# Kernel optimization log

Hardware: AMD Instinct MI355X
Metric: run time of the kernel (lower is better)

The kernel has to match this reference:

```python
import jax, jax.numpy as jnp
import numpy as np

D = 2048
H = 16
KV = 4
DH = D // H  # 128
REP = H // KV
ROPE_BASE = 10000.0


def _rope(x, pos):
    # x: (B, h, L, Dh), pos: (L,)
    half = x.shape[-1] // 2
    inv_freq = 1.0 / (ROPE_BASE ** (jnp.arange(0, half, dtype=jnp.float32) / half))
    ang = pos.astype(jnp.float32)[:, None] * inv_freq[None, :]          # (L, half)
    cos = jnp.concatenate([jnp.cos(ang), jnp.cos(ang)], axis=-1)        # (L, Dh)
    sin = jnp.concatenate([jnp.sin(ang), jnp.sin(ang)], axis=-1)
    x1, x2 = x[..., :half], x[..., half:]
    rot = jnp.concatenate([-x2, x1], axis=-1)
    return x * cos[None, None] + rot * sin[None, None]


def setup_inputs() -> dict:
    key = jax.random.key(0)
    ks = jax.random.split(key, 5)
    s = 1.0 / np.sqrt(D)
    return {
        "x": jax.random.normal(ks[0], (2, 2048, D), dtype=jnp.float32),
        "wq": jax.random.uniform(ks[1], (H * DH, D), jnp.float32, -s, s),
        "wk": jax.random.uniform(ks[2], (KV * DH, D), jnp.float32, -s, s),
        "wv": jax.random.uniform(ks[3], (KV * DH, D), jnp.float32, -s, s),
        "wo": jax.random.uniform(ks[4], (D, H * DH), jnp.float32, -s, s),
    }


def reference(x, wq, wk, wv, wo):
    B, T, _ = x.shape
    q = (x @ wq.T).reshape(B, T, H, DH).transpose(0, 2, 1, 3)    # (B,H,T,Dh)
    k = (x @ wk.T).reshape(B, T, KV, DH).transpose(0, 2, 1, 3)   # (B,KV,T,Dh)
    v = (x @ wv.T).reshape(B, T, KV, DH).transpose(0, 2, 1, 3)
    Tc = T  # no kv cache
    pos = jnp.arange(Tc)
    q = _rope(q, pos)
    k = _rope(k, pos)
    # GQA: repeat kv heads to match query heads
    k_full = jnp.repeat(k, REP, axis=1)                          # (B,H,Tc,Dh)
    v_full = jnp.repeat(v, REP, axis=1)
    scale = 1.0 / np.sqrt(DH)
    scores = jnp.einsum('bhtd,bhsd->bhts', q, k_full) * scale    # (B,H,T,Tc)
    row = jnp.arange(T)[:, None]
    col = jnp.arange(Tc)[None, :]
    causal = col <= row + (Tc - T)
    scores = jnp.where(causal[None, None], scores, -jnp.inf)
    attn = jax.nn.softmax(scores, axis=-1)
    out = jnp.einsum('bhts,bhsd->bhtd', attn, v_full)            # (B,H,T,Dh)
    out = out.transpose(0, 2, 1, 3).reshape(B, T, H * DH)
    return out @ wo.T
```

## Files before the change

kernel.cpp:

```cpp
#include <hip/hip_runtime.h>

typedef float f32x4 __attribute__((ext_vector_type(4)));
typedef short s16x8 __attribute__((ext_vector_type(8)));
typedef unsigned short u16;

__device__ __forceinline__ u16 f2bf(float f) {
    union { float f; unsigned u; } v; v.f = f;
    return (u16)((v.u + 0x7fffu + ((v.u >> 16) & 1u)) >> 16);
}
__device__ __forceinline__ float bf2f(u16 h) {
    union { unsigned u; float f; } v; v.u = ((unsigned)h) << 16;
    return v.f;
}
__device__ __forceinline__ float fast_exp2(float x) {
#if __has_builtin(__builtin_amdgcn_exp2f)
    return __builtin_amdgcn_exp2f(x);
#else
    return exp2f(x);
#endif
}

__device__ __forceinline__ void gload_lds16(const void* g, void* l) {
    __builtin_amdgcn_global_load_lds((__attribute__((address_space(1))) void*)g,
                                     (__attribute__((address_space(3))) void*)l, 16, 0, 0);
}

__global__ __launch_bounds__(256) void cvt_all(const float* __restrict__ x,  const float* __restrict__ wq,
                                               const float* __restrict__ wk, const float* __restrict__ wv,
                                               u16* __restrict__ xb, u16* __restrict__ wqkvb) {
    int u = blockIdx.x * 256 + threadIdx.x;
    const float* src;
    u16* dst;
    if (u < 1048576) { src = x + (size_t)u * 8; dst = xb + (size_t)u * 8; }
    else {
        int w = u - 1048576;
        dst = wqkvb + (size_t)w * 8;
        if (w < 524288)      src = wq + (size_t)w * 8;
        else if (w < 655360) src = wk + (size_t)(w - 524288) * 8;
        else                 src = wv + (size_t)(w - 655360) * 8;
    }
    const float4* p = (const float4*)src;
    float4 a = p[0], b = p[1];
    s16x8 o;
    o[0] = f2bf(a.x); o[1] = f2bf(a.y); o[2] = f2bf(a.z); o[3] = f2bf(a.w);
    o[4] = f2bf(b.x); o[5] = f2bf(b.y); o[6] = f2bf(b.z); o[7] = f2bf(b.w);
    *(s16x8*)dst = o;
}

__global__ __launch_bounds__(256) void cvt_kernel(const float* __restrict__ in,
                                                  u16* __restrict__ out, int n8) {
    int i = blockIdx.x * 256 + threadIdx.x;
    if (i >= n8) return;
    const float4* p = (const float4*)(in + (size_t)i * 8);
    float4 a = p[0], b = p[1];
    s16x8 o;
    o[0] = f2bf(a.x); o[1] = f2bf(a.y); o[2] = f2bf(a.z); o[3] = f2bf(a.w);
    o[4] = f2bf(b.x); o[5] = f2bf(b.y); o[6] = f2bf(b.z); o[7] = f2bf(b.w);
    *(s16x8*)(out + (size_t)i * 8) = o;
}

template<int OUT>
__global__ __launch_bounds__(256) void gemm128(const u16* __restrict__ A, const u16* __restrict__ B,
                                               void* __restrict__ C, void* __restrict__ Ck,
                                               void* __restrict__ Cv, int M, int N, int K) {
    __shared__ __align__(16) u16 Ald[128 * 64];
    __shared__ __align__(16) u16 Bld[128 * 64];
    const int t = threadIdx.x, wid = t >> 6, lane = t & 63;
    const int m0 = blockIdx.y * 128, n0 = blockIdx.x * 128;
    const int ml = lane & 15, quad = lane >> 4, m7 = ml & 7;
    const int wm = (wid & 1) * 64, wn = (wid >> 1) * 64;
    const int sr = lane >> 3, sc = lane & 7;

    f32x4 acc[4][4] = {};

    for (int k0 = 0; k0 < K; k0 += 64) {
        if (k0) __syncthreads();
        #pragma unroll
        for (int i = 0; i < 4; ++i) {
            int seg = wid * 4 + i;
            int r = seg * 8 + sr;
            int c = (sc ^ (r & 7)) * 8;
            gload_lds16(A + (size_t)(m0 + r) * K + k0 + c, &Ald[seg * 512]);
            gload_lds16(B + (size_t)(n0 + r) * K + k0 + c, &Bld[seg * 512]);
        }
        __syncthreads();
        #pragma unroll
        for (int kk = 0; kk < 64; kk += 32) {
            s16x8 af[4], bf[4];
            #pragma unroll
            for (int mi = 0; mi < 4; ++mi)
                af[mi] = *(const s16x8*)&Ald[(wm + mi * 16 + ml) * 64 + (((kk >> 3) + quad) ^ m7) * 8];
            #pragma unroll
            for (int ni = 0; ni < 4; ++ni)
                bf[ni] = *(const s16x8*)&Bld[(wn + ni * 16 + ml) * 64 + (((kk >> 3) + quad) ^ m7) * 8];
            #pragma unroll
            for (int mi = 0; mi < 4; ++mi)
                #pragma unroll
                for (int ni = 0; ni < 4; ++ni)
                    acc[mi][ni] = __builtin_amdgcn_mfma_f32_16x16x32_bf16(af[mi], bf[ni], acc[mi][ni], 0, 0, 0);
        }
    }
    #pragma unroll
    for (int mi = 0; mi < 4; ++mi)
        #pragma unroll
        for (int ni = 0; ni < 4; ++ni) {
            int gmb = m0 + wm + mi * 16 + quad * 4;
            int gn  = n0 + wn + ni * 16 + ml;
            if constexpr (OUT == 4) {
                if (n0 < 2048) {
                    #pragma unroll
                    for (int r = 0; r < 4; ++r)
                        ((u16*)C)[(size_t)(gmb + r) * 2048 + gn] = f2bf(acc[mi][ni][r]);
                } else if (n0 < 2560) {
                    #pragma unroll
                    for (int r = 0; r < 4; ++r)
                        ((u16*)Ck)[(size_t)(gmb + r) * 512 + (gn - 2048)] = f2bf(acc[mi][ni][r]);
                } else {
                    ushort4 v;
                    v.x = f2bf(acc[mi][ni][0]); v.y = f2bf(acc[mi][ni][1]);
                    v.z = f2bf(acc[mi][ni][2]); v.w = f2bf(acc[mi][ni][3]);
                    *(ushort4*)((u16*)Cv + (size_t)(gn - 2560) * M + gmb) = v;
                }
            } else {
                #pragma unroll
                for (int r = 0; r < 4; ++r)
                    ((float*)C)[(size_t)(gmb + r) * N + gn] = acc[mi][ni][r];
            }
        }
}

__global__ __launch_bounds__(256) void rope_kernel(u16* __restrict__ qb, u16* __restrict__ kb,
                                                   int nq, int ntot, float sq) {
    int idx = blockIdx.x * 256 + threadIdx.x;
    if (idx >= ntot) return;
    u16* base; int nheads; float scl; int id;
    if (idx < nq) { base = qb; nheads = 16; scl = sq;  id = idx; }
    else          { base = kb; nheads = 4;  scl = 1.f; id = idx - nq; }
    int i = id & 63;
    int rest = id >> 6;
    int hh = rest % nheads;
    int tok = rest / nheads;
    int tpos = tok & 2047;
    u16* row = base + (size_t)tok * nheads * 128 + hh * 128;
    float x1 = bf2f(row[i]);
    float x2 = bf2f(row[i + 64]);
    float inv = expf(-(float)i * 0.14391156731570787f);
    float ang = (float)tpos * inv;
    float s, c;
    sincosf(ang, &s, &c);
    row[i]      = f2bf((x1 * c - x2 * s) * scl);
    row[i + 64] = f2bf((x2 * c + x1 * s) * scl);
}

__global__ __launch_bounds__(256, 2) void attn_kernel(const u16* __restrict__ Q, const u16* __restrict__ Kb,
                                                      const u16* __restrict__ Vt, u16* __restrict__ O) {
    __shared__ __align__(16) u16 Klds[64 * 128];
    __shared__ __align__(16) u16 Vlds[128 * 64];
    __shared__ __align__(16) u16 Plds[4][2][16 * 64];
    const int t = threadIdx.x, wslot = t >> 6, lane = t & 63;
    const int qa = blockIdx.x, qb = 127 - (int)blockIdx.x;
    const int kv = blockIdx.y, b = blockIdx.z;
    const int h = kv * 4 + wslot;
    const int ml = lane & 15, quad = lane >> 4, m7 = ml & 7;
    const int t0a = qa * 16, t0b = qb * 16;

    s16x8 qfA[4], qfB[4];
    {
        const u16* qpA = Q + ((size_t)(b * 2048 + t0a + ml) * 2048 + h * 128);
        const u16* qpB = Q + ((size_t)(b * 2048 + t0b + ml) * 2048 + h * 128);
        #pragma unroll
        for (int kc = 0; kc < 4; ++kc) {
            qfA[kc] = *(const s16x8*)(qpA + kc * 32 + quad * 8);
            qfB[kc] = *(const s16x8*)(qpB + kc * 32 + quad * 8);
        }
    }

    s16x8 ones;
    #pragma unroll
    for (int j = 0; j < 8; ++j) ones[j] = (short)0x3F80;

    f32x4 OA[8] = {}, OB[8] = {};
    f32x4 LA = {}, LB = {};

    const int nsb = (qb >> 2) + 1;
    const int lastA = qa >> 2;

    for (int it = 0; it < nsb; ++it) {
        const int s0 = it * 64;
        if (it) __syncthreads();
        #pragma unroll
        for (int i = 0; i < 4; ++i) {
            int seg = wslot * 4 + i;
            int kr = seg * 4 + (lane >> 4);
            int kc = ((lane & 15) ^ (kr & 7)) * 8;
            gload_lds16(Kb + (size_t)(b * 2048 + s0 + kr) * 512 + kv * 128 + kc, &Klds[seg * 512]);
            int vr = seg * 8 + (lane >> 3);
            int vc = ((lane & 7) ^ (vr & 7)) * 8;
            gload_lds16(Vt + (size_t)(kv * 128 + vr) * 4096 + b * 2048 + s0 + vc, &Vlds[seg * 512]);
        }
        __syncthreads();

        const bool actA = (it <= lastA);

        f32x4 Sa[4] = {}, Sb[4] = {};
        if (actA) {
            #pragma unroll
            for (int kc = 0; kc < 4; ++kc)
                #pragma unroll
                for (int ti = 0; ti < 4; ++ti) {
                    s16x8 kf = *(const s16x8*)&Klds[(ti * 16 + ml) * 128 + ((kc * 4 + quad) ^ m7) * 8];
                    Sb[ti] = __builtin_amdgcn_mfma_f32_16x16x32_bf16(qfB[kc], kf, Sb[ti], 0, 0, 0);
                    Sa[ti] = __builtin_amdgcn_mfma_f32_16x16x32_bf16(qfA[kc], kf, Sa[ti], 0, 0, 0);
                }
        } else {
            #pragma unroll
            for (int kc = 0; kc < 4; ++kc)
                #pragma unroll
                for (int ti = 0; ti < 4; ++ti) {
                    s16x8 kf = *(const s16x8*)&Klds[(ti * 16 + ml) * 128 + ((kc * 4 + quad) ^ m7) * 8];
                    Sb[ti] = __builtin_amdgcn_mfma_f32_16x16x32_bf16(qfB[kc], kf, Sb[ti], 0, 0, 0);
                }
        }

        auto do_soft = [&](f32x4* S, int t0, int pslot) {
            u16* pl = &Plds[wslot][pslot][0];
            #pragma unroll
            for (int r = 0; r < 4; ++r) {
                int qr = t0 + quad * 4 + r;
                int row = quad * 4 + r;
                #pragma unroll
                for (int ti = 0; ti < 4; ++ti) {
                    float e = fast_exp2(S[ti][r]);
                    if (s0 + ti * 16 + ml > qr) e = 0.f;
                    union { float f; unsigned u; } cv; cv.f = e;
                    pl[row * 64 + (((ti * 2 + (ml >> 3)) ^ (row & 7)) * 8) + (ml & 7)] = (u16)(cv.u >> 16);
                }
            }
        };
        do_soft(Sb, t0b, 1);
        if (actA) do_soft(Sa, t0a, 0);
        asm volatile("s_waitcnt lgkmcnt(0)" ::: "memory");
        s16x8 pfA[2], pfB[2];
        pfB[0] = *(const s16x8*)&Plds[wslot][1][ml * 64 + ((quad)     ^ m7) * 8];
        pfB[1] = *(const s16x8*)&Plds[wslot][1][ml * 64 + ((4 + quad) ^ m7) * 8];
        if (actA) {
            pfA[0] = *(const s16x8*)&Plds[wslot][0][ml * 64 + ((quad)     ^ m7) * 8];
            pfA[1] = *(const s16x8*)&Plds[wslot][0][ml * 64 + ((4 + quad) ^ m7) * 8];
        }
        asm volatile("s_waitcnt lgkmcnt(0)" ::: "memory");

        if (actA) {
            #pragma unroll
            for (int c = 0; c < 2; ++c) {
                #pragma unroll
                for (int nt = 0; nt < 8; ++nt) {
                    s16x8 vf = *(const s16x8*)&Vlds[(nt * 16 + ml) * 64 + ((c * 4 + quad) ^ m7) * 8];
                    OB[nt] = __builtin_amdgcn_mfma_f32_16x16x32_bf16(pfB[c], vf, OB[nt], 0, 0, 0);
                    OA[nt] = __builtin_amdgcn_mfma_f32_16x16x32_bf16(pfA[c], vf, OA[nt], 0, 0, 0);
                }
                LB = __builtin_amdgcn_mfma_f32_16x16x32_bf16(pfB[c], ones, LB, 0, 0, 0);
                LA = __builtin_amdgcn_mfma_f32_16x16x32_bf16(pfA[c], ones, LA, 0, 0, 0);
            }
        } else {
            #pragma unroll
            for (int c = 0; c < 2; ++c) {
                #pragma unroll
                for (int nt = 0; nt < 8; ++nt) {
                    s16x8 vf = *(const s16x8*)&Vlds[(nt * 16 + ml) * 64 + ((c * 4 + quad) ^ m7) * 8];
                    OB[nt] = __builtin_amdgcn_mfma_f32_16x16x32_bf16(pfB[c], vf, OB[nt], 0, 0, 0);
                }
                LB = __builtin_amdgcn_mfma_f32_16x16x32_bf16(pfB[c], ones, LB, 0, 0, 0);
            }
        }
    }

    #pragma unroll
    for (int nt = 0; nt < 8; ++nt)
        #pragma unroll
        for (int r = 0; r < 4; ++r) {
            int col = h * 128 + nt * 16 + ml;
            O[(size_t)(b * 2048 + t0b + quad * 4 + r) * 2048 + col] = f2bf(OB[nt][r] / LB[r]);
            O[(size_t)(b * 2048 + t0a + quad * 4 + r) * 2048 + col] = f2bf(OA[nt][r] / LA[r]);
        }
}

extern "C" void kernel_launch(void* const* d_in, const int* in_sizes, int n_in,
                              void* d_out, int out_size, void* d_ws, size_t ws_size,
                              hipStream_t stream) {
    const float* x  = (const float*)d_in[0];
    const float* wq = (const float*)d_in[1];
    const float* wk = (const float*)d_in[2];
    const float* wv = (const float*)d_in[3];
    const float* wo = (const float*)d_in[4];
    float* out = (float*)d_out;
    char* ws = (char*)d_ws;

    const size_t MB = 1024 * 1024;
    u16* xb    = (u16*)(ws);
    u16* qb    = (u16*)(ws + 16 * MB);
    u16* kb    = (u16*)(ws + 32 * MB);
    u16* vtb   = (u16*)(ws + 36 * MB);
    u16* wqkvb = (u16*)(ws + 40 * MB);
    u16* ab    = xb;
    u16* wob   = wqkvb;

    cvt_all<<<7168, 256, 0, stream>>>(x, wq, wk, wv, xb, wqkvb);

    gemm128<4><<<dim3(24, 32), 256, 0, stream>>>(xb, wqkvb, qb, kb, vtb, 4096, 3072, 2048);

    cvt_kernel<<<2048, 256, 0, stream>>>(wo, wob, 524288);

    rope_kernel<<<20480, 256, 0, stream>>>(qb, kb, 4194304, 5242880, 0.12751743f);

    attn_kernel<<<dim3(64, 4, 2), 256, 0, stream>>>(qb, kb, vtb, ab);

    gemm128<1><<<dim3(16, 32), 256, 0, stream>>>(ab, wob, out, nullptr, nullptr, 4096, 2048, 2048);
}
```

Measured before the change: 342.3 us.

## Double-buffer K/V tiles with smaller key blocks and two-head workgroups in attention

The attention kernel now runs two heads per 128-thread workgroup instead of four per 256-thread workgroup, doubling the grid along the head axis. Key blocks shrink from 64 to 32 and K/V tiles are double-buffered, so the next block's global-to-LDS load is issued before the current block is computed, overlapping load latency with MFMA work. Causal masking is now applied only on the diagonal block. Each K/V tile is loaded by twice as many workgroups and each takes more loop iterations, which adds sync overhead and reduces reuse.

After: 397.9 us. 16.3% more time.

```diff
diff --git a/kernel.cpp b/kernel.cpp
--- a/kernel.cpp
+++ b/kernel.cpp
@@ -152,17 +152,17 @@
     row[i + 64] = f2bf((x2 * c + x1 * s) * scl);
 }
 
-__global__ __launch_bounds__(256, 2) void attn_kernel(const u16* __restrict__ Q, const u16* __restrict__ Kb,
+__global__ __launch_bounds__(128, 4) void attn_kernel(const u16* __restrict__ Q, const u16* __restrict__ Kb,
                                                       const u16* __restrict__ Vt, u16* __restrict__ O) {
-    __shared__ __align__(16) u16 Klds[64 * 128];
-    __shared__ __align__(16) u16 Vlds[128 * 64];
-    __shared__ __align__(16) u16 Plds[4][2][16 * 64];
+    __shared__ __align__(16) u16 Klds[2][32 * 128];
+    __shared__ __align__(16) u16 Vlds[2][128 * 32];
+    __shared__ __align__(16) u16 Plds[2][2][16 * 32];
     const int t = threadIdx.x, wslot = t >> 6, lane = t & 63;
-    const int qa = blockIdx.x, qb = 127 - (int)blockIdx.x;
-    const int kv = blockIdx.y, b = blockIdx.z;
-    const int h = kv * 4 + wslot;
-    const int ml = lane & 15, quad = lane >> 4, m7 = ml & 7;
-    const int t0a = qa * 16, t0b = qb * 16;
+    const int qa = blockIdx.x, qbt = 127 - (int)blockIdx.x;
+    const int kv = blockIdx.y >> 1, hgrp = blockIdx.y & 1, b = blockIdx.z;
+    const int h = kv * 4 + hgrp * 2 + wslot;
+    const int ml = lane & 15, quad = lane >> 4, m3 = ml & 3;
+    const int t0a = qa * 16, t0b = qbt * 16;
 
     s16x8 qfA[4], qfB[4];
     {
@@ -182,33 +182,45 @@
     f32x4 OA[8] = {}, OB[8] = {};
     f32x4 LA = {}, LB = {};
 
-    const int nsb = (qb >> 2) + 1;
-    const int lastA = qa >> 2;
-
-    for (int it = 0; it < nsb; ++it) {
-        const int s0 = it * 64;
-        if (it) __syncthreads();
+    const int La = (t0a >> 5) + 1;
+    const int Lb = (t0b >> 5) + 1;
+
+    auto stage = [&](int bi, int c) {
+        const int s0 = c * 32;
         #pragma unroll
         for (int i = 0; i < 4; ++i) {
-            int seg = wslot * 4 + i;
-            int kr = seg * 4 + (lane >> 4);
-            int kc = ((lane & 15) ^ (kr & 7)) * 8;
-            gload_lds16(Kb + (size_t)(b * 2048 + s0 + kr) * 512 + kv * 128 + kc, &Klds[seg * 512]);
-            int vr = seg * 8 + (lane >> 3);
-            int vc = ((lane & 7) ^ (vr & 7)) * 8;
-            gload_lds16(Vt + (size_t)(kv * 128 + vr) * 4096 + b * 2048 + s0 + vc, &Vlds[seg * 512]);
-        }
+            int kseg = wslot * 4 + i;
+            int krow = kseg * 4 + (lane >> 4);
+            int kch  = (lane & 15) ^ (krow & 7);
+            gload_lds16(Kb + (size_t)(b * 2048 + s0 + krow) * 512 + kv * 128 + kch * 8,
+                        &Klds[bi][kseg * 512]);
+            int vseg = wslot * 4 + i;
+            int vrow = vseg * 16 + (lane >> 2);
+            int vch  = (lane & 3) ^ (vrow & 3);
+            gload_lds16(Vt + (size_t)(kv * 128 + vrow) * 4096 + b * 2048 + s0 + vch * 8,
+                        &Vlds[bi][vseg * 512]);
+        }
+    };
+
+    stage(0, 0);
+
+    for (int c = 0; c < Lb; ++c) {
         __syncthreads();
-
-        const bool actA = (it <= lastA);
-
-        f32x4 Sa[4] = {}, Sb[4] = {};
+        if (c + 1 < Lb) stage((c + 1) & 1, c + 1);
+        const u16* kl = Klds[c & 1];
+        const u16* vl = Vlds[c & 1];
+        const int s0 = c * 32;
+        const bool actA  = (c < La);
+        const bool maskA = (c == La - 1);
+        const bool maskB = (c == Lb - 1);
+
+        f32x4 Sa[2] = {}, Sb[2] = {};
         if (actA) {
             #pragma unroll
             for (int kc = 0; kc < 4; ++kc)
                 #pragma unroll
-                for (int ti = 0; ti < 4; ++ti) {
-                    s16x8 kf = *(const s16x8*)&Klds[(ti * 16 + ml) * 128 + ((kc * 4 + quad) ^ m7) * 8];
+                for (int ti = 0; ti < 2; ++ti) {
+                    s16x8 kf = *(const s16x8*)&kl[(ti * 16 + ml) * 128 + (((kc * 4 + quad) ^ (ml & 7)) * 8)];
                     Sb[ti] = __builtin_amdgcn_mfma_f32_16x16x32_bf16(qfB[kc], kf, Sb[ti], 0, 0, 0);
                     Sa[ti] = __builtin_amdgcn_mfma_f32_16x16x32_bf16(qfA[kc], kf, Sa[ti], 0, 0, 0);
                 }
@@ -216,61 +228,51 @@
             #pragma unroll
             for (int kc = 0; kc < 4; ++kc)
                 #pragma unroll
-                for (int ti = 0; ti < 4; ++ti) {
-                    s16x8 kf = *(const s16x8*)&Klds[(ti * 16 + ml) * 128 + ((kc * 4 + quad) ^ m7) * 8];
+                for (int ti = 0; ti < 2; ++ti) {
+                    s16x8 kf = *(const s16x8*)&kl[(ti * 16 + ml) * 128 + (((kc * 4 + quad) ^ (ml & 7)) * 8)];
                     Sb[ti] = __builtin_amdgcn_mfma_f32_16x16x32_bf16(qfB[kc], kf, Sb[ti], 0, 0, 0);
                 }
         }
 
-        auto do_soft = [&](f32x4* S, int t0, int pslot) {
+        auto do_soft = [&](f32x4* S, int t0, int pslot, bool msk) {
             u16* pl = &Plds[wslot][pslot][0];
             #pragma unroll
             for (int r = 0; r < 4; ++r) {
-                int qr = t0 + quad * 4 + r;
                 int row = quad * 4 + r;
-                #pragma unroll
-                for (int ti = 0; ti < 4; ++ti) {
+                int qr = t0 + row;
+                #pragma unroll
+                for (int ti = 0; ti < 2; ++ti) {
                     float e = fast_exp2(S[ti][r]);
-                    if (s0 + ti * 16 + ml > qr) e = 0.f;
+                    if (msk && (s0 + ti * 16 + ml > qr)) e = 0.f;
                     union { float f; unsigned u; } cv; cv.f = e;
-                    pl[row * 64 + (((ti * 2 + (ml >> 3)) ^ (row & 7)) * 8) + (ml & 7)] = (u16)(cv.u >> 16);
+                    pl[row * 32 + (((ti * 2 + (ml >> 3)) ^ (row & 3)) * 8) + (ml & 7)] = (u16)(cv.u >> 16);
                 }
             }
         };
-        do_soft(Sb, t0b, 1);
-        if (actA) do_soft(Sa, t0a, 0);
+        do_soft(Sb, t0b, 1, maskB);
+        if (actA) do_soft(Sa, t0a, 0, maskA);
         asm volatile("s_waitcnt lgkmcnt(0)" ::: "memory");
-        s16x8 pfA[2], pfB[2];
-        pfB[0] = *(const s16x8*)&Plds[wslot][1][ml * 64 + ((quad)     ^ m7) * 8];
-        pfB[1] = *(const s16x8*)&Plds[wslot][1][ml * 64 + ((4 + quad) ^ m7) * 8];
+        s16x8 pfA, pfB;
+        pfB = *(const s16x8*)&Plds[wslot][1][ml * 32 + ((quad ^ m3) * 8)];
+        if (actA) pfA = *(const s16x8*)&Plds[wslot][0][ml * 32 + ((quad ^ m3) * 8)];
+        asm volatile("s_waitcnt lgkmcnt(0)" ::: "memory");
+
         if (actA) {
-            pfA[0] = *(const s16x8*)&Plds[wslot][0][ml * 64 + ((quad)     ^ m7) * 8];
-            pfA[1] = *(const s16x8*)&Plds[wslot][0][ml * 64 + ((4 + quad) ^ m7) * 8];
-        }
-        asm volatile("s_waitcnt lgkmcnt(0)" ::: "memory");
-
-        if (actA) {
-            #pragma unroll
-            for (int c = 0; c < 2; ++c) {
-                #pragma unroll
-                for (int nt = 0; nt < 8; ++nt) {
-                    s16x8 vf = *(const s16x8*)&Vlds[(nt * 16 + ml) * 64 + ((c * 4 + quad) ^ m7) * 8];
-                    OB[nt] = __builtin_amdgcn_mfma_f32_16x16x32_bf16(pfB[c], vf, OB[nt], 0, 0, 0);
-                    OA[nt] = __builtin_amdgcn_mfma_f32_16x16x32_bf16(pfA[c], vf, OA[nt], 0, 0, 0);
-                }
-                LB = __builtin_amdgcn_mfma_f32_16x16x32_bf16(pfB[c], ones, LB, 0, 0, 0);
-                LA = __builtin_amdgcn_mfma_f32_16x16x32_bf16(pfA[c], ones, LA, 0, 0, 0);
+            #pragma unroll
+            for (int nt = 0; nt < 8; ++nt) {
+                s16x8 vf = *(const s16x8*)&vl[(nt * 16 + ml) * 32 + ((quad ^ m3) * 8)];
+                OB[nt] = __builtin_amdgcn_mfma_f32_16x16x32_bf16(pfB, vf, OB[nt], 0, 0, 0);
+                OA[nt] = __builtin_amdgcn_mfma_f32_16x16x32_bf16(pfA, vf, OA[nt], 0, 0, 0);
             }
+            LB = __builtin_amdgcn_mfma_f32_16x16x32_bf16(pfB, ones, LB, 0, 0, 0);
+            LA = __builtin_amdgcn_mfma_f32_16x16x32_bf16(pfA, ones, LA, 0, 0, 0);
         } else {
             #pragma unroll
-            for (int c = 0; c < 2; ++c) {
-                #pragma unroll
-                for (int nt = 0; nt < 8; ++nt) {
-                    s16x8 vf = *(const s16x8*)&Vlds[(nt * 16 + ml) * 64 + ((c * 4 + quad) ^ m7) * 8];
-                    OB[nt] = __builtin_amdgcn_mfma_f32_16x16x32_bf16(pfB[c], vf, OB[nt], 0, 0, 0);
-                }
-                LB = __builtin_amdgcn_mfma_f32_16x16x32_bf16(pfB[c], ones, LB, 0, 0, 0);
+            for (int nt = 0; nt < 8; ++nt) {
+                s16x8 vf = *(const s16x8*)&vl[(nt * 16 + ml) * 32 + ((quad ^ m3) * 8)];
+                OB[nt] = __builtin_amdgcn_mfma_f32_16x16x32_bf16(pfB, vf, OB[nt], 0, 0, 0);
             }
+            LB = __builtin_amdgcn_mfma_f32_16x16x32_bf16(pfB, ones, LB, 0, 0, 0);
         }
     }
 
@@ -312,7 +314,7 @@
 
     rope_kernel<<<20480, 256, 0, stream>>>(qb, kb, 4194304, 5242880, 0.12751743f);
 
-    attn_kernel<<<dim3(64, 4, 2), 256, 0, stream>>>(qb, kb, vtb, ab);
+    attn_kernel<<<dim3(64, 8, 2), 128, 0, stream>>>(qb, kb, vtb, ab);
 
     gemm128<1><<<dim3(16, 32), 256, 0, stream>>>(ab, wob, out, nullptr, nullptr, 4096, 2048, 2048);
 }
```

## Double-buffer K tiles in LDS and overlap V/K loads with QK compute

Applied to the files above, without the earlier changes.

K gets two LDS buffers, and the first tile is loaded before the loop. Each iteration issues the V load for the current tile and prefetches the next K tile, then computes QK^T and softmax. A second barrier before the PV MFMAs makes sure V has landed. The aim is to hide global-to-LDS latency behind the score computation. The cost is more LDS per block and an extra barrier per iteration, and that barrier may also wait on the K prefetch, which limits the overlap.

Measured after the change: 348.1 us. Within noise of the previous version (+1.7%).

```diff
diff --git a/kernel.cpp b/kernel.cpp
--- a/kernel.cpp
+++ b/kernel.cpp
@@ -154,15 +154,15 @@
 
 __global__ __launch_bounds__(256, 2) void attn_kernel(const u16* __restrict__ Q, const u16* __restrict__ Kb,
                                                       const u16* __restrict__ Vt, u16* __restrict__ O) {
-    __shared__ __align__(16) u16 Klds[64 * 128];
+    __shared__ __align__(16) u16 Klds[2][64 * 128];
     __shared__ __align__(16) u16 Vlds[128 * 64];
     __shared__ __align__(16) u16 Plds[4][2][16 * 64];
     const int t = threadIdx.x, wslot = t >> 6, lane = t & 63;
-    const int qa = blockIdx.x, qb = 127 - (int)blockIdx.x;
+    const int qa = blockIdx.x, qbt = 127 - (int)blockIdx.x;
     const int kv = blockIdx.y, b = blockIdx.z;
     const int h = kv * 4 + wslot;
     const int ml = lane & 15, quad = lane >> 4, m7 = ml & 7;
-    const int t0a = qa * 16, t0b = qb * 16;
+    const int t0a = qa * 16, t0b = qbt * 16;
 
     s16x8 qfA[4], qfB[4];
     {
@@ -182,24 +182,39 @@
     f32x4 OA[8] = {}, OB[8] = {};
     f32x4 LA = {}, LB = {};
 
-    const int nsb = (qb >> 2) + 1;
+    const int nsb = (qbt >> 2) + 1;
     const int lastA = qa >> 2;
 
-    for (int it = 0; it < nsb; ++it) {
-        const int s0 = it * 64;
-        if (it) __syncthreads();
+    auto stageK = [&](int bi, int c) {
+        const int s0 = c * 64;
         #pragma unroll
         for (int i = 0; i < 4; ++i) {
             int seg = wslot * 4 + i;
             int kr = seg * 4 + (lane >> 4);
             int kc = ((lane & 15) ^ (kr & 7)) * 8;
-            gload_lds16(Kb + (size_t)(b * 2048 + s0 + kr) * 512 + kv * 128 + kc, &Klds[seg * 512]);
+            gload_lds16(Kb + (size_t)(b * 2048 + s0 + kr) * 512 + kv * 128 + kc, &Klds[bi][seg * 512]);
+        }
+    };
+    auto stageV = [&](int c) {
+        const int s0 = c * 64;
+        #pragma unroll
+        for (int i = 0; i < 4; ++i) {
+            int seg = wslot * 4 + i;
             int vr = seg * 8 + (lane >> 3);
             int vc = ((lane & 7) ^ (vr & 7)) * 8;
             gload_lds16(Vt + (size_t)(kv * 128 + vr) * 4096 + b * 2048 + s0 + vc, &Vlds[seg * 512]);
         }
+    };
+
+    stageK(0, 0);
+
+    for (int it = 0; it < nsb; ++it) {
+        const int s0 = it * 64;
         __syncthreads();
-
+        stageV(it);
+        if (it + 1 < nsb) stageK((it + 1) & 1, it + 1);
+
+        const u16* kl = Klds[it & 1];
         const bool actA = (it <= lastA);
 
         f32x4 Sa[4] = {}, Sb[4] = {};
@@ -208,7 +223,7 @@
             for (int kc = 0; kc < 4; ++kc)
                 #pragma unroll
                 for (int ti = 0; ti < 4; ++ti) {
-                    s16x8 kf = *(const s16x8*)&Klds[(ti * 16 + ml) * 128 + ((kc * 4 + quad) ^ m7) * 8];
+                    s16x8 kf = *(const s16x8*)&kl[(ti * 16 + ml) * 128 + ((kc * 4 + quad) ^ m7) * 8];
                     Sb[ti] = __builtin_amdgcn_mfma_f32_16x16x32_bf16(qfB[kc], kf, Sb[ti], 0, 0, 0);
                     Sa[ti] = __builtin_amdgcn_mfma_f32_16x16x32_bf16(qfA[kc], kf, Sa[ti], 0, 0, 0);
                 }
@@ -217,7 +232,7 @@
             for (int kc = 0; kc < 4; ++kc)
                 #pragma unroll
                 for (int ti = 0; ti < 4; ++ti) {
-                    s16x8 kf = *(const s16x8*)&Klds[(ti * 16 + ml) * 128 + ((kc * 4 + quad) ^ m7) * 8];
+                    s16x8 kf = *(const s16x8*)&kl[(ti * 16 + ml) * 128 + ((kc * 4 + quad) ^ m7) * 8];
                     Sb[ti] = __builtin_amdgcn_mfma_f32_16x16x32_bf16(qfB[kc], kf, Sb[ti], 0, 0, 0);
                 }
         }
@@ -249,6 +264,8 @@
         }
         asm volatile("s_waitcnt lgkmcnt(0)" ::: "memory");
 
+        __syncthreads();
+
         if (actA) {
             #pragma unroll
             for (int c = 0; c < 2; ++c) {
```
